# Performance work log

Hardware: AMD Instinct MI355X
Metric: run time of the kernel (lower is better)

## Reference

```python
import jax, jax.numpy as jnp
import numpy as np
from jax import lax

EPS_LN = 1e-5
EPS_NORM = 1e-12


def _layernorm_c(x, w, b):
    # WithBias LayerNorm over channel dim of NCHW (equivalent to to_3d -> LN(-1) -> to_4d)
    mu = jnp.mean(x, axis=1, keepdims=True)
    var = jnp.mean(jnp.square(x - mu), axis=1, keepdims=True)
    return (x - mu) / jnp.sqrt(var + EPS_LN) * w[None, :, None, None] + b[None, :, None, None]


def _conv1x1(x, w):
    # w: [O, C] ; x: [B, C, H, W]
    return jnp.einsum('oc,bchw->bohw', w, x)


def _dwconv3x3(x, w):
    # w: [C, 1, 3, 3], depthwise, padding=1
    C = x.shape[1]
    return lax.conv_general_dilated(
        x, w, window_strides=(1, 1), padding=((1, 1), (1, 1)),
        dimension_numbers=('NCHW', 'OIHW', 'NCHW'), feature_group_count=C)


def setup_inputs() -> dict:
    key = jax.random.key(0)
    ks = jax.random.split(key, 8)
    B, C, H, W = 4, 384, 128, 128
    n_heads = 8
    s = 1.0 / np.sqrt(C)
    inp = {
        'x': jax.random.normal(ks[0], (B, C, H, W), jnp.float32),
        'wq': jax.random.normal(ks[1], (C, C), jnp.float32) * s,
        'wk': jax.random.normal(ks[2], (C, C), jnp.float32) * s,
        'wv': jax.random.normal(ks[3], (C, C), jnp.float32) * s,
        'dwq': jax.random.normal(ks[4], (C, 1, 3, 3), jnp.float32) * (1.0 / 3.0),
        'dwk': jax.random.normal(ks[5], (C, 1, 3, 3), jnp.float32) * (1.0 / 3.0),
        'dwv': jax.random.normal(ks[6], (C, 1, 3, 3), jnp.float32) * (1.0 / 3.0),
        'scale': jnp.ones((n_heads, 1, 1), jnp.float32),
        'ln1_w': jnp.ones((C,), jnp.float32),
        'ln1_b': jnp.zeros((C,), jnp.float32),
        'ln2_w': jnp.ones((C,), jnp.float32),
        'ln2_b': jnp.zeros((C,), jnp.float32),
    }
    return inp


def reference(x, wq, wk, wv, dwq, dwk, dwv, scale, ln1_w, ln1_b, ln2_w, ln2_b):
    B, C, H, W = x.shape
    n_heads = scale.shape[0]
    d = C // n_heads
    L = H * W

    x_norm = _layernorm_c(x, ln1_w, ln1_b)
    q = _dwconv3x3(_conv1x1(x_norm, wq), dwq)
    k = _dwconv3x3(_conv1x1(x_norm, wk), dwk)
    v = _dwconv3x3(_conv1x1(x_norm, wv), dwv)

    # b (n d) h w -> b n d L
    q = q.reshape(B, n_heads, d, L)
    k = k.reshape(B, n_heads, d, L)
    v = v.reshape(B, n_heads, d, L)

    # L2-normalize over spatial dim (F.normalize, eps=1e-12)
    q = q / jnp.maximum(jnp.linalg.norm(q, axis=-1, keepdims=True), EPS_NORM)
    k = k / jnp.maximum(jnp.linalg.norm(k, axis=-1, keepdims=True), EPS_NORM)

    # channel (transposed) attention: [b, n, d, d]
    attn = jnp.einsum('bndl,bnel->bnde', q, k) * scale[None]
    attn = jax.nn.softmax(attn, axis=-1)
    out = jnp.einsum('bnde,bnel->bndl', attn, v)

    out = out.reshape(B, C, H, W)
    return _layernorm_c(out, ln2_w, ln2_b)
```

## Files before the change

### kernel.cpp

```cpp
#include <hip/hip_runtime.h>
#include <hip/hip_bf16.h>
#include <stdint.h>

#define B_ 4
#define C_ 384
#define H_ 128
#define W_ 128
#define L_ (H_*W_)
#define NH 8
#define DH 48
#define SPLIT 8

typedef __attribute__((ext_vector_type(8))) short bf16x8;
typedef __attribute__((ext_vector_type(4))) float f32x4;
typedef unsigned short u16;
typedef unsigned int u32;

__device__ __forceinline__ float bf2f(u16 v){
  union { float f; u32 u; } x; x.u = ((u32)v) << 16; return x.f;
}
__device__ __forceinline__ u16 f2bf(float f){
  __hip_bfloat16 h = __float2bfloat16(f);
  return *reinterpret_cast<u16*>(&h);
}

#define GLOAD_LDS16(g, l) \
  __builtin_amdgcn_global_load_lds((const __attribute__((address_space(1))) u32*)(g), \
                                   (__attribute__((address_space(3))) u32*)(l), 16, 0, 0)

__global__ __launch_bounds__(256) void k_cvt_w(const float* __restrict__ wq,
                                               const float* __restrict__ wk,
                                               const float* __restrict__ wv,
                                               u16* __restrict__ wc){
  int i = blockIdx.x * 256 + threadIdx.x;
  if (i >= 3*C_*C_) return;
  int m = i / C_;
  int c = i - m*C_;
  const float* src = (m < C_) ? wq : (m < 2*C_) ? wk : wv;
  int mm = (m >= 2*C_) ? m - 2*C_ : (m >= C_) ? m - C_ : m;
  wc[i] = f2bf(src[mm*C_ + c]);
}

__global__ __launch_bounds__(256) void k_ln1(const float* __restrict__ x,
                                             const float* __restrict__ w,
                                             const float* __restrict__ b,
                                             u16* __restrict__ xt){
  const int tid = threadIdx.x;
  const int bb = blockIdx.x >> 8;
  const int l0 = (blockIdx.x & 255) << 6;
  const int pg = tid >> 4;
  const int cg = tid & 15;
  const int c0 = cg * 24;
  const float* xp = x + (size_t)bb*C_*L_ + (size_t)c0*L_ + l0 + pg*4;

  f32x4 vals[24];
  #pragma unroll
  for (int ci = 0; ci < 24; ++ci)
    vals[ci] = *reinterpret_cast<const f32x4*>(xp + (size_t)ci*L_);

  f32x4 s = {0.f,0.f,0.f,0.f}, s2 = {0.f,0.f,0.f,0.f};
  #pragma unroll
  for (int ci = 0; ci < 24; ++ci){ s += vals[ci]; s2 += vals[ci]*vals[ci]; }
  #pragma unroll
  for (int m = 1; m < 16; m <<= 1){
    #pragma unroll
    for (int r = 0; r < 4; ++r){
      s[r]  += __shfl_xor(s[r],  m);
      s2[r] += __shfl_xor(s2[r], m);
    }
  }
  f32x4 mu, rstd;
  #pragma unroll
  for (int r = 0; r < 4; ++r){
    mu[r]   = s[r] * (1.f/C_);
    rstd[r] = rsqrtf(s2[r]*(1.f/C_) - mu[r]*mu[r] + 1e-5f);
  }

  u16* dst = xt + ((size_t)bb*L_ + l0 + pg*4)*C_ + c0;
  #pragma unroll
  for (int j = 0; j < 3; ++j){
    f32x4 w0 = *reinterpret_cast<const f32x4*>(w + c0 + j*8);
    f32x4 w1 = *reinterpret_cast<const f32x4*>(w + c0 + j*8 + 4);
    f32x4 b0 = *reinterpret_cast<const f32x4*>(b + c0 + j*8);
    f32x4 b1 = *reinterpret_cast<const f32x4*>(b + c0 + j*8 + 4);
    #pragma unroll
    for (int pp = 0; pp < 4; ++pp){
      uint4 pk;
      u16* tp = reinterpret_cast<u16*>(&pk);
      #pragma unroll
      for (int e = 0; e < 4; ++e)
        tp[e]   = f2bf((vals[j*8+e][pp]   - mu[pp]) * rstd[pp] * w0[e] + b0[e]);
      #pragma unroll
      for (int e = 0; e < 4; ++e)
        tp[4+e] = f2bf((vals[j*8+4+e][pp] - mu[pp]) * rstd[pp] * w1[e] + b1[e]);
      *reinterpret_cast<uint4*>(dst + (size_t)pp*C_ + j*8) = pk;
    }
  }
}

#define SLOTA (128*32)
#define SLOTB (256*32)
__global__ __launch_bounds__(512) void k_gemm(const u16* __restrict__ Wc,
                                              const u16* __restrict__ Xt,
                                              u16* __restrict__ qkv){
  __shared__ u16 As[3*SLOTA];
  __shared__ u16 Bs[3*SLOTB];
  const int tid = threadIdx.x;
  const int wg = (int)blockIdx.x;
  const int lin = (wg & 7) * 288 + (wg >> 3);
  const int bm = lin % 9;
  const int bn = lin / 9;
  const int m0 = bm * 128;
  const int n0 = bn * 256;
  const int w = tid >> 6, lane = tid & 63;
  const int wm = (w >> 2) * 64, wn = (w & 3) * 64;
  const int fr = lane & 15, kqi = lane >> 4;
  const int sslot = kqi ^ ((fr >> 1) & 3);

  f32x4 acc[4][4] = {};

#define STAGE(slot, k0) do { \
    { int rowA_ = tid >> 2, qA_ = tid & 3; \
      int qsA_ = qA_ ^ ((rowA_ >> 1) & 3); \
      GLOAD_LDS16(Wc + (size_t)(m0+rowA_)*384 + (k0) + qsA_*8, As + (slot)*SLOTA + tid*8); } \
    _Pragma("unroll") \
    for (int i_ = 0; i_ < 2; ++i_){ \
      int idx_ = i_*512 + tid; \
      int row_ = idx_ >> 2, q_ = idx_ & 3; \
      int qs_ = q_ ^ ((row_ >> 1) & 3); \
      GLOAD_LDS16(Xt + (size_t)(n0+row_)*384 + (k0) + qs_*8, Bs + (slot)*SLOTB + idx_*8); \
    } } while(0)

  STAGE(0, 0);
  STAGE(1, 32);

  #pragma unroll
  for (int it = 0; it < 12; ++it){
    const int cur = it % 3;
    __builtin_amdgcn_sched_barrier(0);
    if (it < 11) asm volatile("s_waitcnt vmcnt(3)" ::: "memory");
    else         asm volatile("s_waitcnt vmcnt(0)" ::: "memory");
    __builtin_amdgcn_sched_barrier(0);
    __builtin_amdgcn_s_barrier();
    __builtin_amdgcn_sched_barrier(0);
    if (it + 2 < 12) STAGE((it+2)%3, (it+2)*32);

    const u16* Ab = As + cur*SLOTA;
    const u16* Bb = Bs + cur*SLOTB;
    bf16x8 af[4], bfm[4];
    #pragma unroll
    for (int i = 0; i < 4; ++i)
      af[i] = *reinterpret_cast<const bf16x8*>(Ab + (wm + i*16 + fr)*32 + sslot*8);
    #pragma unroll
    for (int j = 0; j < 4; ++j)
      bfm[j] = *reinterpret_cast<const bf16x8*>(Bb + (wn + j*16 + fr)*32 + sslot*8);
    #pragma unroll
    for (int i = 0; i < 4; ++i)
      #pragma unroll
      for (int j = 0; j < 4; ++j)
        acc[i][j] = __builtin_amdgcn_mfma_f32_16x16x32_bf16(af[i], bfm[j], acc[i][j], 0, 0, 0);
  }
#undef STAGE

  #pragma unroll
  for (int i = 0; i < 4; ++i){
    int mbase = m0 + wm + i*16 + (lane >> 4) * 4;
    #pragma unroll
    for (int j = 0; j < 4; ++j){
      int n = n0 + wn + j*16 + fr;
      int bb = n >> 14, l = n & (L_-1);
      #pragma unroll
      for (int r = 0; r < 4; ++r){
        int m = mbase + r;
        int proj = (m >= 2*C_) ? 2 : (m >= C_) ? 1 : 0;
        int c = m - proj*C_;
        qkv[(((size_t)proj*B_ + bb)*C_ + c)*L_ + l] = f2bf(acc[i][j][r]);
      }
    }
  }
}

__global__ __launch_bounds__(256) void k_dwconv(u16* __restrict__ qkv,
                                                const float* __restrict__ dwq,
                                                const float* __restrict__ dwk,
                                                const float* __restrict__ dwv,
                                                float* __restrict__ sumsq){
  __shared__ u16 pl[128*128];
  int pid = blockIdx.x;
  int t = pid / (B_*C_);
  int bc = pid - t*(B_*C_);
  int c = bc % C_;
  const float* dw = ((t == 0) ? dwq : (t == 1) ? dwk : dwv) + c*9;
  u16* plane = qkv + ((size_t)t*B_*C_ + bc) * L_;
  int tid = threadIdx.x;
  #pragma unroll
  for (int i = 0; i < 8; ++i){
    int idx = i*256 + tid;
    GLOAD_LDS16(plane + idx*8, pl + idx*8);
  }
  float wgt[9];
  #pragma unroll
  for (int i = 0; i < 9; ++i) wgt[i] = dw[i];
  asm volatile("s_waitcnt vmcnt(0)" ::: "memory");
  __syncthreads();

  const int tx = tid & 15;
  const int ty = tid >> 4;
  const int lane = tid & 63;
  const int y0 = ty*8;

  float rv[3][8], rl[3], rr_[3];
  float ss = 0.f;

  #pragma unroll
  for (int i = 0; i < 10; ++i){
    const int sl = i % 3;
    int r = y0 - 1 + i;
    int rc = (r < 0) ? 0 : (r > 127 ? 127 : r);
    uint4 pk = *reinterpret_cast<const uint4*>(pl + rc*128 + tx*8);
    const u16* e = reinterpret_cast<const u16*>(&pk);
    bool oob = (r < 0) || (r > 127);
    #pragma unroll
    for (int k = 0; k < 8; ++k)
      rv[sl][k] = oob ? 0.f : bf2f(e[k]);
    float lft = __shfl(rv[sl][7], lane - 1);
    float rgt = __shfl(rv[sl][0], lane + 1);
    rl[sl]  = (tx == 0)  ? 0.f : lft;
    rr_[sl] = (tx == 15) ? 0.f : rgt;

    if (i >= 2){
      const int sa = (i-2) % 3, sb = (i-1) % 3, sc = i % 3;
      const int y = i - 2;
      float o[8];
      #pragma unroll
      for (int xx = 0; xx < 8; ++xx){
        float am1 = (xx == 0) ? rl[sa]  : rv[sa][xx-1];
        float ap1 = (xx == 7) ? rr_[sa] : rv[sa][xx+1];
        float bm1 = (xx == 0) ? rl[sb]  : rv[sb][xx-1];
        float bp1 = (xx == 7) ? rr_[sb] : rv[sb][xx+1];
        float cm1 = (xx == 0) ? rl[sc]  : rv[sc][xx-1];
        float cp1 = (xx == 7) ? rr_[sc] : rv[sc][xx+1];
        float a = wgt[0]*am1 + wgt[1]*rv[sa][xx] + wgt[2]*ap1
                + wgt[3]*bm1 + wgt[4]*rv[sb][xx] + wgt[5]*bp1
                + wgt[6]*cm1 + wgt[7]*rv[sc][xx] + wgt[8]*cp1;
        o[xx] = a;
        ss += a * a;
      }
      uint4 st;
      u16* sp = reinterpret_cast<u16*>(&st);
      #pragma unroll
      for (int xx = 0; xx < 8; ++xx) sp[xx] = f2bf(o[xx]);
      *reinterpret_cast<uint4*>(plane + (y0 + y)*128 + tx*8) = st;
    }
  }

  if (t < 2){
    #pragma unroll
    for (int off = 32; off > 0; off >>= 1) ss += __shfl_down(ss, off);
    __shared__ float red[4];
    if ((tid & 63) == 0) red[tid >> 6] = ss;
    __syncthreads();
    if (tid == 0) sumsq[t*(B_*C_) + bc] = red[0] + red[1] + red[2] + red[3];
  }
}

__global__ __launch_bounds__(512) void k_qk(const u16* __restrict__ qkv,
                                            float* __restrict__ Spart){
  int gid = blockIdx.x;
  int s = gid / (B_*NH);
  int bn = gid - s*(B_*NH);
  int b = bn / NH, n = bn - b*NH;
  const u16* qb = qkv + ((size_t)b*C_ + n*DH) * L_;
  const u16* kb = qkv + ((size_t)B_*C_ + (size_t)b*C_ + n*DH) * L_;
  int tid = threadIdx.x, w = tid >> 6, lane = tid & 63;
  int fr = lane & 15, kq = (lane >> 4) * 8;
  int l0 = s * (L_/SPLIT) + w * (L_/SPLIT/8);
  f32x4 acc[3][3] = {};
  #pragma unroll
  for (int kk = 0; kk < (L_/SPLIT/8); kk += 32){
    int koff = l0 + kk + kq;
    bf16x8 af[3], bfm[3];
    #pragma unroll
    for (int i = 0; i < 3; ++i) af[i]  = *reinterpret_cast<const bf16x8*>(qb + (size_t)(i*16+fr)*L_ + koff);
    #pragma unroll
    for (int j = 0; j < 3; ++j) bfm[j] = *reinterpret_cast<const bf16x8*>(kb + (size_t)(j*16+fr)*L_ + koff);
    #pragma unroll
    for (int i = 0; i < 3; ++i)
      #pragma unroll
      for (int j = 0; j < 3; ++j)
        acc[i][j] = __builtin_amdgcn_mfma_f32_16x16x32_bf16(af[i], bfm[j], acc[i][j], 0, 0, 0);
  }
  __shared__ float red[8*2304];
  float* rw = red + w*2304;
  #pragma unroll
  for (int i = 0; i < 3; ++i)
    #pragma unroll
    for (int j = 0; j < 3; ++j)
      #pragma unroll
      for (int r = 0; r < 4; ++r){
        int row = i*16 + (lane >> 4)*4 + r;
        int col = j*16 + fr;
        rw[row*48 + col] = acc[i][j][r];
      }
  __syncthreads();
  float* dst = Spart + ((size_t)gid) * 2304;
  for (int idx = tid; idx < 2304; idx += 512){
    float a = 0.f;
    #pragma unroll
    for (int ww = 0; ww < 8; ++ww) a += red[ww*2304 + idx];
    dst[idx] = a;
  }
}

__global__ void k_softmax(const float* __restrict__ Spart,
                          const float* __restrict__ sumsq,
                          const float* __restrict__ scale,
                          u16* __restrict__ attn96){
  int bn = blockIdx.x;
  int b = bn / NH, n = bn - b*NH;
  int i = threadIdx.x;
  if (i >= DH) return;
  const float* sq = sumsq + (size_t)b*C_ + n*DH;
  const float* sk = sumsq + (size_t)B_*C_ + (size_t)b*C_ + n*DH;
  float nq = fmaxf(sqrtf(sq[i]), 1e-12f);
  float sc = scale[n];
  float row[48];
  #pragma unroll
  for (int j = 0; j < DH; ++j){
    float acc = 0.f;
    #pragma unroll
    for (int s = 0; s < SPLIT; ++s)
      acc += Spart[((size_t)(s*(B_*NH) + bn))*2304 + i*48 + j];
    float nk = fmaxf(sqrtf(sk[j]), 1e-12f);
    row[j] = acc / (nq * nk) * sc;
  }
  float m = row[0];
  #pragma unroll
  for (int j = 1; j < DH; ++j) m = fmaxf(m, row[j]);
  float sum = 0.f;
  #pragma unroll
  for (int j = 0; j < DH; ++j){ row[j] = __expf(row[j] - m); sum += row[j]; }
  float inv = 1.f / sum;
  u16* dst = attn96 + ((size_t)bn)*DH*96 + i*96;
  #pragma unroll
  for (int j = 0; j < DH; ++j){
    float a = row[j] * inv;
    u16 hi = f2bf(a);
    float lo = a - bf2f(hi);
    dst[j]      = hi;
    dst[48 + j] = f2bf(lo);
  }
}

#define VT_STRIDE 784
__device__ __forceinline__ int vt_off(int p, int ch){
  return p*VT_STRIDE + ((p>>3)<<4) + 2*ch;
}
__global__ __launch_bounds__(256) void k_av_ln2(const u16* __restrict__ qkv,
                                                const u16* __restrict__ attn96,
                                                const float* __restrict__ w2,
                                                const float* __restrict__ b2,
                                                float* __restrict__ out){
  __shared__ u16 vt[(64*VT_STRIDE + 8*16)/2];
  char* vtb = reinterpret_cast<char*>(vt);
  const int tid = threadIdx.x;
  const int bb = blockIdx.x >> 8;
  const int l0 = (blockIdx.x & 255) << 6;
  const u16* vg = qkv + ((size_t)2*B_*C_ + (size_t)bb*C_)*L_ + l0;

  #pragma unroll
  for (int it = 0; it < 6; ++it){
    int idx = it*256 + tid;
    int cp = idx >> 3, g = idx & 7;
    int c = cp*2;
    uint4 p0 = *reinterpret_cast<const uint4*>(vg + (size_t)c*L_ + g*8);
    uint4 p1 = *reinterpret_cast<const uint4*>(vg + (size_t)(c+1)*L_ + g*8);
    const u16* e0 = reinterpret_cast<const u16*>(&p0);
    const u16* e1 = reinterpret_cast<const u16*>(&p1);
    #pragma unroll
    for (int j = 0; j < 8; ++j){
      int p = g*8 + j;
      u32 packed = ((u32)e0[j]) | (((u32)e1[j]) << 16);
      *reinterpret_cast<u32*>(vtb + vt_off(p, c)) = packed;
    }
  }
  __syncthreads();

  const int w = tid >> 6, lane = tid & 63;
  const int fr = lane & 15, kq = (lane >> 4) * 8;
  const int prow = w*16;
  f32x4 acc[24];
  #pragma unroll
  for (int j = 0; j < 24; ++j) acc[j] = (f32x4){0.f,0.f,0.f,0.f};

  const u16* ab = attn96 + ((size_t)bb*NH)*DH*96;
  #pragma unroll
  for (int n = 0; n < NH; ++n){
    bf16x8 af[3];
    #pragma unroll
    for (int s = 0; s < 3; ++s){
      int ep = s*32 + kq;
      int ch = n*DH + (ep >= 48 ? ep - 48 : ep);
      af[s] = *reinterpret_cast<const bf16x8*>(vtb + vt_off(prow + fr, ch));
    }
    #pragma unroll
    for (int jj = 0; jj < 3; ++jj){
      const u16* arow = ab + ((size_t)n*DH + jj*16 + fr)*96;
      #pragma unroll
      for (int s = 0; s < 3; ++s){
        bf16x8 bf = *reinterpret_cast<const bf16x8*>(arow + s*32 + kq);
        acc[n*3+jj] = __builtin_amdgcn_mfma_f32_16x16x32_bf16(af[s], bf, acc[n*3+jj], 0, 0, 0);
      }
    }
  }

  f32x4 s = {0.f,0.f,0.f,0.f}, s2 = {0.f,0.f,0.f,0.f};
  #pragma unroll
  for (int j = 0; j < 24; ++j){ s += acc[j]; s2 += acc[j]*acc[j]; }
  #pragma unroll
  for (int m = 1; m < 16; m <<= 1){
    #pragma unroll
    for (int r = 0; r < 4; ++r){
      s[r]  += __shfl_xor(s[r],  m);
      s2[r] += __shfl_xor(s2[r], m);
    }
  }
  f32x4 mu, rstd;
  #pragma unroll
  for (int r = 0; r < 4; ++r){
    mu[r]   = s[r] * (1.f/C_);
    rstd[r] = rsqrtf(s2[r]*(1.f/C_) - mu[r]*mu[r] + 1e-5f);
  }
  const int pbase = l0 + prow + (lane>>4)*4;
  #pragma unroll
  for (int j = 0; j < 24; ++j){
    int c = j*16 + fr;
    float wc = w2[c], bc = b2[c];
    f32x4 o;
    #pragma unroll
    for (int r = 0; r < 4; ++r)
      o[r] = (acc[j][r] - mu[r]) * rstd[r] * wc + bc;
    *reinterpret_cast<f32x4*>(out + ((size_t)bb*C_ + c)*L_ + pbase) = o;
  }
}

extern "C" void kernel_launch(void* const* d_in, const int* in_sizes, int n_in,
                              void* d_out, int out_size, void* d_ws, size_t ws_size,
                              hipStream_t stream){
  const float* x     = (const float*)d_in[0];
  const float* wq    = (const float*)d_in[1];
  const float* wk    = (const float*)d_in[2];
  const float* wv    = (const float*)d_in[3];
  const float* dwq   = (const float*)d_in[4];
  const float* dwk   = (const float*)d_in[5];
  const float* dwv   = (const float*)d_in[6];
  const float* scale = (const float*)d_in[7];
  const float* ln1w  = (const float*)d_in[8];
  const float* ln1b  = (const float*)d_in[9];
  const float* ln2w  = (const float*)d_in[10];
  const float* ln2b  = (const float*)d_in[11];
  float* out = (float*)d_out;

  char* ws = (char*)d_ws;
  u16*   qkv    = (u16*)ws;
  u16*   xt     = (u16*)(ws + 150994944);
  u16*   wc     = (u16*)(ws + 201326592);
  float* sumsq  = (float*)(ws + 202211328);
  float* Spart  = (float*)(ws + 202223616);
  u16*   attn96 = (u16*)(ws + 204582912);

  k_cvt_w  <<<1728, 256, 0, stream>>>(wq, wk, wv, wc);
  k_ln1    <<<1024, 256, 0, stream>>>(x, ln1w, ln1b, xt);
  k_gemm   <<<2304, 512, 0, stream>>>(wc, xt, qkv);
  k_dwconv <<<3*B_*C_, 256, 0, stream>>>(qkv, dwq, dwk, dwv, sumsq);
  k_qk     <<<SPLIT*B_*NH, 512, 0, stream>>>(qkv, Spart);
  k_softmax<<<B_*NH, 64, 0, stream>>>(Spart, sumsq, scale, attn96);
  k_av_ln2 <<<1024, 256, 0, stream>>>(qkv, attn96, ln2w, ln2b, out);
}
```

Baseline: 264.4 us.

## Widen GEMM K-tile to 64 with 8-way swizzle and fuse weight-convert into LN1

The QKV GEMM now stages 64-wide K slices instead of 32 in its triple-buffered LDS pipeline. That halves the number of main-loop barriers and waits, and switches to an 8-chunk XOR swizzle to avoid LDS bank conflicts. Each stage runs two MFMA sub-steps with raised wave priority and an intermediate barrier. The separate weight-conversion kernel is merged into the LN1 kernel as extra blocks, removing one launch. The larger tiles double LDS use (144KB per block), which may lower occupancy.

Measured after the change: 271.7 us. +2.8%, slower.

```diff
diff --git a/kernel.cpp b/kernel.cpp
--- a/kernel.cpp
+++ b/kernel.cpp
@@ -28,23 +28,25 @@
   __builtin_amdgcn_global_load_lds((const __attribute__((address_space(1))) u32*)(g), \
                                    (__attribute__((address_space(3))) u32*)(l), 16, 0, 0)
 
-__global__ __launch_bounds__(256) void k_cvt_w(const float* __restrict__ wq,
-                                               const float* __restrict__ wk,
-                                               const float* __restrict__ wv,
-                                               u16* __restrict__ wc){
-  int i = blockIdx.x * 256 + threadIdx.x;
-  if (i >= 3*C_*C_) return;
-  int m = i / C_;
-  int c = i - m*C_;
-  const float* src = (m < C_) ? wq : (m < 2*C_) ? wk : wv;
-  int mm = (m >= 2*C_) ? m - 2*C_ : (m >= C_) ? m - C_ : m;
-  wc[i] = f2bf(src[mm*C_ + c]);
-}
-
-__global__ __launch_bounds__(256) void k_ln1(const float* __restrict__ x,
-                                             const float* __restrict__ w,
-                                             const float* __restrict__ b,
-                                             u16* __restrict__ xt){
+__global__ __launch_bounds__(256) void k_prep(const float* __restrict__ x,
+                                              const float* __restrict__ w,
+                                              const float* __restrict__ b,
+                                              u16* __restrict__ xt,
+                                              const float* __restrict__ wq,
+                                              const float* __restrict__ wk,
+                                              const float* __restrict__ wv,
+                                              u16* __restrict__ wc){
+  if ((int)blockIdx.x >= 1024){
+    int i = ((int)blockIdx.x - 1024) * 256 + threadIdx.x;
+    if (i < 3*C_*C_){
+      int m = i / C_;
+      int c = i - m*C_;
+      const float* src = (m < C_) ? wq : (m < 2*C_) ? wk : wv;
+      int mm = (m >= 2*C_) ? m - 2*C_ : (m >= C_) ? m - C_ : m;
+      wc[i] = f2bf(src[mm*C_ + c]);
+    }
+    return;
+  }
   const int tid = threadIdx.x;
   const int bb = blockIdx.x >> 8;
   const int l0 = (blockIdx.x & 255) << 6;
@@ -98,8 +100,8 @@
   }
 }
 
-#define SLOTA (128*32)
-#define SLOTB (256*32)
+#define SLOTA (128*64)
+#define SLOTB (256*64)
 __global__ __launch_bounds__(512) void k_gemm(const u16* __restrict__ Wc,
                                               const u16* __restrict__ Xt,
                                               u16* __restrict__ qkv){
@@ -115,50 +117,65 @@
   const int w = tid >> 6, lane = tid & 63;
   const int wm = (w >> 2) * 64, wn = (w & 3) * 64;
   const int fr = lane & 15, kqi = lane >> 4;
-  const int sslot = kqi ^ ((fr >> 1) & 3);
 
   f32x4 acc[4][4] = {};
 
 #define STAGE(slot, k0) do { \
-    { int rowA_ = tid >> 2, qA_ = tid & 3; \
-      int qsA_ = qA_ ^ ((rowA_ >> 1) & 3); \
-      GLOAD_LDS16(Wc + (size_t)(m0+rowA_)*384 + (k0) + qsA_*8, As + (slot)*SLOTA + tid*8); } \
     _Pragma("unroll") \
-    for (int i_ = 0; i_ < 2; ++i_){ \
-      int idx_ = i_*512 + tid; \
-      int row_ = idx_ >> 2, q_ = idx_ & 3; \
-      int qs_ = q_ ^ ((row_ >> 1) & 3); \
+    for (int a_ = 0; a_ < 2; ++a_){ \
+      int idx_ = a_*512 + tid; \
+      int row_ = idx_ >> 3, q_ = idx_ & 7; \
+      int qs_ = q_ ^ (row_ & 7); \
+      GLOAD_LDS16(Wc + (size_t)(m0+row_)*384 + (k0) + qs_*8, As + (slot)*SLOTA + idx_*8); \
+    } \
+    _Pragma("unroll") \
+    for (int b_ = 0; b_ < 4; ++b_){ \
+      int idx_ = b_*512 + tid; \
+      int row_ = idx_ >> 3, q_ = idx_ & 7; \
+      int qs_ = q_ ^ (row_ & 7); \
       GLOAD_LDS16(Xt + (size_t)(n0+row_)*384 + (k0) + qs_*8, Bs + (slot)*SLOTB + idx_*8); \
     } } while(0)
 
   STAGE(0, 0);
-  STAGE(1, 32);
-
-  #pragma unroll
-  for (int it = 0; it < 12; ++it){
-    const int cur = it % 3;
+  STAGE(1, 64);
+
+  #pragma unroll
+  for (int t = 0; t < 6; ++t){
+    const int cur = t % 3;
     __builtin_amdgcn_sched_barrier(0);
-    if (it < 11) asm volatile("s_waitcnt vmcnt(3)" ::: "memory");
-    else         asm volatile("s_waitcnt vmcnt(0)" ::: "memory");
+    if (t < 5) asm volatile("s_waitcnt vmcnt(6)" ::: "memory");
+    else       asm volatile("s_waitcnt vmcnt(0)" ::: "memory");
     __builtin_amdgcn_sched_barrier(0);
     __builtin_amdgcn_s_barrier();
     __builtin_amdgcn_sched_barrier(0);
-    if (it + 2 < 12) STAGE((it+2)%3, (it+2)*32);
+    if (t + 2 < 6) STAGE((t+2)%3, (t+2)*64);
+    __builtin_amdgcn_sched_barrier(0);
 
     const u16* Ab = As + cur*SLOTA;
     const u16* Bb = Bs + cur*SLOTB;
-    bf16x8 af[4], bfm[4];
-    #pragma unroll
-    for (int i = 0; i < 4; ++i)
-      af[i] = *reinterpret_cast<const bf16x8*>(Ab + (wm + i*16 + fr)*32 + sslot*8);
-    #pragma unroll
-    for (int j = 0; j < 4; ++j)
-      bfm[j] = *reinterpret_cast<const bf16x8*>(Bb + (wn + j*16 + fr)*32 + sslot*8);
-    #pragma unroll
-    for (int i = 0; i < 4; ++i)
+    #pragma unroll
+    for (int kh = 0; kh < 2; ++kh){
+      bf16x8 af[4], bfm[4];
+      const int ch = ((kh*4 + kqi) ^ (fr & 7)) * 8;
+      #pragma unroll
+      for (int i = 0; i < 4; ++i)
+        af[i] = *reinterpret_cast<const bf16x8*>(Ab + (wm + i*16 + fr)*64 + ch);
       #pragma unroll
       for (int j = 0; j < 4; ++j)
-        acc[i][j] = __builtin_amdgcn_mfma_f32_16x16x32_bf16(af[i], bfm[j], acc[i][j], 0, 0, 0);
+        bfm[j] = *reinterpret_cast<const bf16x8*>(Bb + (wn + j*16 + fr)*64 + ch);
+      __builtin_amdgcn_s_setprio(1);
+      #pragma unroll
+      for (int i = 0; i < 4; ++i)
+        #pragma unroll
+        for (int j = 0; j < 4; ++j)
+          acc[i][j] = __builtin_amdgcn_mfma_f32_16x16x32_bf16(af[i], bfm[j], acc[i][j], 0, 0, 0);
+      __builtin_amdgcn_s_setprio(0);
+      if (kh == 0){
+        __builtin_amdgcn_sched_barrier(0);
+        __builtin_amdgcn_s_barrier();
+        __builtin_amdgcn_sched_barrier(0);
+      }
+    }
   }
 #undef STAGE
 
@@ -469,8 +486,7 @@
   float* Spart  = (float*)(ws + 202223616);
   u16*   attn96 = (u16*)(ws + 204582912);
 
-  k_cvt_w  <<<1728, 256, 0, stream>>>(wq, wk, wv, wc);
-  k_ln1    <<<1024, 256, 0, stream>>>(x, ln1w, ln1b, xt);
+  k_prep   <<<2752, 256, 0, stream>>>(x, ln1w, ln1b, xt, wq, wk, wv, wc);
   k_gemm   <<<2304, 512, 0, stream>>>(wc, xt, qkv);
   k_dwconv <<<3*B_*C_, 256, 0, stream>>>(qkv, dwq, dwk, dwv, sumsq);
   k_qk     <<<SPLIT*B_*NH, 512, 0, stream>>>(qkv, Spart);
```
